# Kernel tuning notes

Hardware: AMD Instinct MI355X
Metric: run time of the kernel (lower is better)

Reference implementation:

```python
import jax, jax.numpy as jnp
import numpy as np

N_NODES = 100000
N_EDGES = 1600000
IN_CH, HID_CH, OUT_CH = 128, 128, 64


def glorot(key, fan_in, fan_out):
    lim = np.sqrt(6.0 / (fan_in + fan_out)).astype(np.float32)
    return jax.random.uniform(key, (fan_in, fan_out), jnp.float32, -lim, lim)


def gcn_conv(x, src, dst, W, b):
    """PyG GCNConv: add self-loops, symmetric deg^-1/2 normalization,
    linear transform, scatter-add aggregation at targets, plus bias."""
    n = x.shape[0]
    xw = x @ W  # [N, F_out]
    loop = jnp.arange(n)
    s = jnp.concatenate([src, loop])  # sources (message origin)
    d = jnp.concatenate([dst, loop])  # targets (aggregation site)
    deg = jax.ops.segment_sum(jnp.ones_like(d, dtype=xw.dtype), d, num_segments=n)
    dinv = jnp.where(deg > 0, jax.lax.rsqrt(deg), 0.0)
    norm = dinv[s] * dinv[d]  # [E+N]
    out = jax.ops.segment_sum(norm[:, None] * xw[s], d, num_segments=n)
    return out + b


def setup_inputs() -> dict:
    key = jax.random.key(0)
    ks = jax.random.split(key, 8)
    x = jax.random.normal(ks[0], (N_NODES, IN_CH), jnp.float32)
    edge_index = jax.random.randint(ks[1], (2, N_EDGES), 0, N_NODES, jnp.int64)
    return {
        "x": x,
        "edge_index": edge_index,
        "W1": glorot(ks[2], IN_CH, HID_CH),
        "b1": jnp.zeros((HID_CH,), jnp.float32),
        "W2": glorot(ks[3], HID_CH, HID_CH),
        "b2": jnp.zeros((HID_CH,), jnp.float32),
        "W3": glorot(ks[4], HID_CH, OUT_CH),
        "b3": jnp.zeros((OUT_CH,), jnp.float32),
    }


def reference(x, edge_index, W1, b1, W2, b2, W3, b3):
    src, dst = edge_index[0], edge_index[1]
    # eval mode: dropout is identity
    h = jax.nn.relu(gcn_conv(x, src, dst, W1, b1))
    h = jax.nn.relu(gcn_conv(h, src, dst, W2, b2))
    h = gcn_conv(h, src, dst, W3, b3)
    return jax.nn.log_softmax(h, axis=1)
```

## Files before the change

kernel.cpp:

```cpp
#include <hip/hip_runtime.h>
#include <math.h>


#define NN 100000
#define NE 1600000
#define NBUK 391
#define BCAP 4608

typedef float floatx4 __attribute__((ext_vector_type(4)));
typedef short short8 __attribute__((ext_vector_type(8)));

__device__ __forceinline__ unsigned short f2bf(float f) {
    unsigned u = __float_as_uint(f);
    unsigned r = (u + 0x7fffu + ((u >> 16) & 1u)) >> 16;
    return (unsigned short)r;
}
__device__ __forceinline__ float bflo(unsigned u) { return __uint_as_float(u << 16); }
__device__ __forceinline__ float bfhi(unsigned u) { return __uint_as_float(u & 0xffff0000u); }

__global__ __launch_bounds__(256) void k_wprep_all(const float* __restrict__ W1, const float* __restrict__ W2,
                                                   const float* __restrict__ W3,
                                                   unsigned short* __restrict__ wt1, unsigned short* __restrict__ wt2,
                                                   unsigned short* __restrict__ wt3) {
    int idx = blockIdx.x * 256 + threadIdx.x;
    if (idx < 16384) {
        int n = idx >> 7, k = idx & 127;
        wt1[idx] = f2bf(W1[k * 128 + n]);
    } else if (idx < 32768) {
        int i = idx - 16384;
        int n = i >> 7, k = i & 127;
        wt2[i] = f2bf(W2[k * 128 + n]);
    } else if (idx < 40960) {
        int i = idx - 32768;
        int n = i >> 7, k = i & 127;
        wt3[i] = f2bf(W3[k * 64 + n]);
    }
}

__global__ __launch_bounds__(256) void k_bucket(const int4* __restrict__ src4, const int4* __restrict__ dst4,
                                                int* __restrict__ bcur, int* __restrict__ bbuf, int E) {
    __shared__ int hist[NBUK];
    __shared__ int base[NBUK];
    int t = threadIdx.x;
    for (int b = t; b < NBUK; b += 256) hist[b] = 0;
    __syncthreads();
    int E4 = E >> 2;
    int q0 = blockIdx.x * 1024;
    int4 sv[4], dv[4];
    bool valid[4];
    #pragma unroll
    for (int j = 0; j < 4; j++) {
        int q = q0 + j * 256 + t;
        valid[j] = (q < E4);
        if (valid[j]) {
            sv[j] = src4[q];
            dv[j] = dst4[q];
            atomicAdd(&hist[dv[j].x >> 8], 1);
            atomicAdd(&hist[dv[j].y >> 8], 1);
            atomicAdd(&hist[dv[j].z >> 8], 1);
            atomicAdd(&hist[dv[j].w >> 8], 1);
        }
    }
    __syncthreads();
    for (int b = t; b < NBUK; b += 256) {
        int c = hist[b];
        base[b] = c ? atomicAdd(&bcur[b], c) : 0;
        hist[b] = 0;
    }
    __syncthreads();
    #pragma unroll
    for (int j = 0; j < 4; j++) {
        if (valid[j]) {
            int ss[4] = {sv[j].x, sv[j].y, sv[j].z, sv[j].w};
            int dd[4] = {dv[j].x, dv[j].y, dv[j].z, dv[j].w};
            #pragma unroll
            for (int u = 0; u < 4; u++) {
                int b = dd[u] >> 8;
                int r = atomicAdd(&hist[b], 1);
                int pos = base[b] + r;
                if (pos < BCAP) bbuf[b * BCAP + pos] = (ss[u] << 8) | (dd[u] & 255);
            }
        }
    }
}

__global__ void k_scanbuckets(const int* __restrict__ bcur, int* __restrict__ bbase, int nb,
                              int* __restrict__ row_ptr, int n, int E) {
    int lane = threadIdx.x;
    int carry = 0;
    for (int base = 0; base < nb; base += 64) {
        int idx = base + lane;
        int v = (idx < nb) ? min(bcur[idx], BCAP) : 0;
        int orig = v;
        #pragma unroll
        for (int o = 1; o < 64; o <<= 1) {
            int u = __shfl_up(v, o);
            if (lane >= o) v += u;
        }
        if (idx < nb) bbase[idx] = carry + v - orig;
        carry += __shfl(v, 63);
    }
    if (lane == 0) row_ptr[n] = E;
}

__global__ __launch_bounds__(256) void k_build(const int* __restrict__ bcur, const int* __restrict__ bbase,
                                               const int* __restrict__ bbuf,
                                               int* __restrict__ row_ptr, int* __restrict__ csr,
                                               float* __restrict__ dinv, int N) {
    __shared__ int sh[256];
    __shared__ int cur[256];
    __shared__ int loc[BCAP];
    int b = blockIdx.x, t = threadIdx.x;
    int cnt = min(bcur[b], BCAP);
    int gbase = bbase[b];
    const int* bp = bbuf + b * BCAP;
    sh[t] = 0;
    __syncthreads();
    for (int i = t; i < cnt; i += 256) atomicAdd(&sh[bp[i] & 255], 1);
    __syncthreads();
    int v = sh[t];
    for (int o = 1; o < 256; o <<= 1) {
        int u = (t >= o) ? sh[t - o] : 0;
        __syncthreads();
        sh[t] += u;
        __syncthreads();
    }
    int excl = sh[t] - v;
    int node = b * 256 + t;
    if (node < N) {
        row_ptr[node] = gbase + excl;
        dinv[node] = rsqrtf((float)v + 1.0f);
    }
    cur[t] = excl;
    __syncthreads();
    for (int i = t; i < cnt; i += 256) {
        int p = bp[i];
        int r = atomicAdd(&cur[p & 255], 1);
        loc[r] = p >> 8;
    }
    __syncthreads();
    for (int i = t; i < cnt; i += 256) csr[gbase + i] = loc[i];
}


template <int NC, bool CVT>
__global__ __launch_bounds__(256) void k_mfma(const void* __restrict__ Av, const unsigned short* __restrict__ Wtg,
                                              const float* __restrict__ dinv, unsigned short* __restrict__ Y, int M) {
    constexpr int K = 128;
    constexpr int NT = NC / 16;
    constexpr int NU = NC / 32;
    __shared__ unsigned short Wt[NC][136];
    __shared__ unsigned short Ost[4][16][NC + 8];
    int t = threadIdx.x;
    for (int idx = t; idx < NC * 16; idx += 256) {
        int nrow = idx >> 4, chunk = idx & 15;
        *(uint4*)&Wt[nrow][chunk * 8] = *(const uint4*)(Wtg + nrow * K + chunk * 8);
    }
    __syncthreads();
    int lane = t & 63, wid = t >> 6;
    int col = lane & 15, quad = lane >> 4;
    int nstrips = M / 16;
    int stride = gridDim.x * 4;
    int s = blockIdx.x * 4 + wid;
    if (s >= nstrips) return;

    auto loadA = [&](int strip, short8 af[4]) {
        int row0 = strip * 16;
        if (CVT) {
            const float* Af = (const float*)Av + (size_t)(row0 + col) * K + quad * 8;
            #pragma unroll
            for (int ks = 0; ks < 4; ks++) {
                float4 f0 = *(const float4*)(Af + ks * 32);
                float4 f1 = *(const float4*)(Af + ks * 32 + 4);
                short8 v;
                v[0] = (short)f2bf(f0.x); v[1] = (short)f2bf(f0.y); v[2] = (short)f2bf(f0.z); v[3] = (short)f2bf(f0.w);
                v[4] = (short)f2bf(f1.x); v[5] = (short)f2bf(f1.y); v[6] = (short)f2bf(f1.z); v[7] = (short)f2bf(f1.w);
                af[ks] = v;
            }
        } else {
            const unsigned short* Ab = (const unsigned short*)Av + (size_t)(row0 + col) * K + quad * 8;
            #pragma unroll
            for (int ks = 0; ks < 4; ks++) af[ks] = *(const short8*)(Ab + ks * 32);
        }
    };

    short8 cur[4];
    loadA(s, cur);
    while (true) {
        int snext = s + stride;
        bool has = (snext < nstrips);
        short8 nxt[4];
        if (has) loadA(snext, nxt);

        floatx4 acc[NT];
        #pragma unroll
        for (int i = 0; i < NT; i++) acc[i] = (floatx4){0.f, 0.f, 0.f, 0.f};
        #pragma unroll
        for (int ks = 0; ks < 4; ks++) {
            #pragma unroll
            for (int nt = 0; nt < NT; nt++) {
                short8 bfrag = *(const short8*)&Wt[nt * 16 + col][ks * 32 + quad * 8];
                acc[nt] = __builtin_amdgcn_mfma_f32_16x16x32_bf16(cur[ks], bfrag, acc[nt], 0, 0, 0);
            }
        }
        int row0 = s * 16;
        #pragma unroll
        for (int r = 0; r < 4; r++) {
            float dv = dinv[row0 + quad * 4 + r];
            #pragma unroll
            for (int nt = 0; nt < NT; nt++)
                Ost[wid][quad * 4 + r][nt * 16 + col] = f2bf(acc[nt][r] * dv);
        }
        #pragma unroll
        for (int i = 0; i < NU; i++) {
            int idx = i * 64 + lane;
            int rr = (NC == 128) ? (idx >> 4) : (idx >> 3);
            int cc = (NC == 128) ? (idx & 15) : (idx & 7);
            ((uint4*)&Y[(size_t)(row0 + rr) * NC])[cc] = *(uint4*)&Ost[wid][rr][cc * 8];
        }
        if (!has) break;
        s = snext;
        #pragma unroll
        for (int ks = 0; ks < 4; ks++) cur[ks] = nxt[ks];
    }
}


__device__ __forceinline__ void acc8(float* a, uint4 v) {
    a[0] += bflo(v.x); a[1] += bfhi(v.x);
    a[2] += bflo(v.y); a[3] += bfhi(v.y);
    a[4] += bflo(v.z); a[5] += bfhi(v.z);
    a[6] += bflo(v.w); a[7] += bfhi(v.w);
}

__global__ __launch_bounds__(256) void k_gather_relu_bf(const uint4* __restrict__ y, const int* __restrict__ csr,
                                                        const int* __restrict__ row_ptr, const float* __restrict__ dinv,
                                                        const float* __restrict__ bias, uint4* __restrict__ h, int n) {
    int half = blockIdx.x & 1;
    int node = (blockIdx.x >> 1) * 32 + (threadIdx.x >> 3);
    int c = (threadIdx.x & 7) + half * 8;
    if (node >= n) return;
    int s0 = row_ptr[node], s1 = row_ptr[node + 1];
    float a[8] = {};
    acc8(a, y[(size_t)node * 16 + c]);
    int p = s0;
    for (; p + 4 <= s1; p += 4) {
        int i0 = csr[p], i1 = csr[p + 1], i2 = csr[p + 2], i3 = csr[p + 3];
        uint4 v0 = y[(size_t)i0 * 16 + c];
        uint4 v1 = y[(size_t)i1 * 16 + c];
        uint4 v2 = y[(size_t)i2 * 16 + c];
        uint4 v3 = y[(size_t)i3 * 16 + c];
        acc8(a, v0); acc8(a, v1); acc8(a, v2); acc8(a, v3);
    }
    for (; p < s1; p++) acc8(a, y[(size_t)csr[p] * 16 + c]);
    float s = dinv[node];
    float4 b0 = ((const float4*)bias)[c * 2];
    float4 b1 = ((const float4*)bias)[c * 2 + 1];
    float r0 = fmaxf(s * a[0] + b0.x, 0.f), r1 = fmaxf(s * a[1] + b0.y, 0.f);
    float r2 = fmaxf(s * a[2] + b0.z, 0.f), r3 = fmaxf(s * a[3] + b0.w, 0.f);
    float r4 = fmaxf(s * a[4] + b1.x, 0.f), r5 = fmaxf(s * a[5] + b1.y, 0.f);
    float r6 = fmaxf(s * a[6] + b1.z, 0.f), r7 = fmaxf(s * a[7] + b1.w, 0.f);
    uint4 o;
    o.x = ((unsigned)f2bf(r1) << 16) | f2bf(r0);
    o.y = ((unsigned)f2bf(r3) << 16) | f2bf(r2);
    o.z = ((unsigned)f2bf(r5) << 16) | f2bf(r4);
    o.w = ((unsigned)f2bf(r7) << 16) | f2bf(r6);
    h[(size_t)node * 16 + c] = o;
}

__global__ __launch_bounds__(256) void k_gather_lsm_bf(const uint4* __restrict__ y, const int* __restrict__ csr,
                                                       const int* __restrict__ row_ptr, const float* __restrict__ dinv,
                                                       const float* __restrict__ bias, float4* __restrict__ out4, int n) {
    int node = blockIdx.x * 32 + (threadIdx.x >> 3);
    int c = threadIdx.x & 7;
    if (node >= n) return;
    int s0 = row_ptr[node], s1 = row_ptr[node + 1];
    float a[8] = {};
    acc8(a, y[(size_t)node * 8 + c]);
    int p = s0;
    for (; p + 4 <= s1; p += 4) {
        int i0 = csr[p], i1 = csr[p + 1], i2 = csr[p + 2], i3 = csr[p + 3];
        uint4 v0 = y[(size_t)i0 * 8 + c];
        uint4 v1 = y[(size_t)i1 * 8 + c];
        uint4 v2 = y[(size_t)i2 * 8 + c];
        uint4 v3 = y[(size_t)i3 * 8 + c];
        acc8(a, v0); acc8(a, v1); acc8(a, v2); acc8(a, v3);
    }
    for (; p < s1; p++) acc8(a, y[(size_t)csr[p] * 8 + c]);
    float s = dinv[node];
    float4 b0 = ((const float4*)bias)[c * 2];
    float4 b1 = ((const float4*)bias)[c * 2 + 1];
    float v[8];
    v[0] = s * a[0] + b0.x; v[1] = s * a[1] + b0.y; v[2] = s * a[2] + b0.z; v[3] = s * a[3] + b0.w;
    v[4] = s * a[4] + b1.x; v[5] = s * a[5] + b1.y; v[6] = s * a[6] + b1.z; v[7] = s * a[7] + b1.w;
    float m = v[0];
    #pragma unroll
    for (int i = 1; i < 8; i++) m = fmaxf(m, v[i]);
    #pragma unroll
    for (int o = 4; o > 0; o >>= 1) m = fmaxf(m, __shfl_xor(m, o));
    float sum = 0.f;
    #pragma unroll
    for (int i = 0; i < 8; i++) sum += expf(v[i] - m);
    #pragma unroll
    for (int o = 4; o > 0; o >>= 1) sum += __shfl_xor(sum, o);
    float lse = m + logf(sum);
    out4[(size_t)node * 16 + c * 2]     = make_float4(v[0] - lse, v[1] - lse, v[2] - lse, v[3] - lse);
    out4[(size_t)node * 16 + c * 2 + 1] = make_float4(v[4] - lse, v[5] - lse, v[6] - lse, v[7] - lse);
}


extern "C" void kernel_launch(void* const* d_in, const int* in_sizes, int n_in,
                              void* d_out, int out_size, void* d_ws, size_t ws_size,
                              hipStream_t stream) {
    const float* x  = (const float*)d_in[0];
    const int*   ei = (const int*)d_in[1];
    const float* W1 = (const float*)d_in[2];
    const float* b1 = (const float*)d_in[3];
    const float* W2 = (const float*)d_in[4];
    const float* b2 = (const float*)d_in[5];
    const float* W3 = (const float*)d_in[6];
    const float* b3 = (const float*)d_in[7];
    float* out = (float*)d_out;

    const int N = NN, E = NE;

    char* ws = (char*)d_ws;
    size_t off = 0;
    auto alloc = [&](size_t bytes) -> void* {
        void* p = ws + off;
        off += bytes;
        off = (off + 255) & ~(size_t)255;
        return p;
    };
    int*            row_ptr = (int*)alloc((size_t)(N + 1) * 4);
    float*          dinvv   = (float*)alloc((size_t)N * 4);
    int*            bcur    = (int*)alloc(512 * 4);
    int*            bbase   = (int*)alloc(512 * 4);
    int*            bbuf    = (int*)alloc((size_t)NBUK * BCAP * 4);
    int*            csr     = (int*)alloc((size_t)E * 4);
    unsigned short* wt1     = (unsigned short*)alloc(128 * 128 * 2);
    unsigned short* wt2     = (unsigned short*)alloc(128 * 128 * 2);
    unsigned short* wt3     = (unsigned short*)alloc(64 * 128 * 2);
    unsigned short* yb      = (unsigned short*)alloc((size_t)N * 128 * 2);
    unsigned short* hb      = (unsigned short*)alloc((size_t)N * 128 * 2);
    (void)ws_size; (void)in_sizes; (void)n_in; (void)out_size;

    const int* srcp = ei;
    const int* dstp = ei + E;

    hipMemsetAsync(bcur, 0, 512 * 4, stream);
    k_wprep_all<<<160, 256, 0, stream>>>(W1, W2, W3, wt1, wt2, wt3);
    k_bucket<<<(E + 4095) / 4096, 256, 0, stream>>>((const int4*)srcp, (const int4*)dstp, bcur, bbuf, E);
    k_scanbuckets<<<1, 64, 0, stream>>>(bcur, bbase, NBUK, row_ptr, N, E);
    k_build<<<NBUK, 256, 0, stream>>>(bcur, bbase, bbuf, row_ptr, csr, dinvv, N);

    k_mfma<128, true><<<768, 256, 0, stream>>>(x, wt1, dinvv, yb, N);
    k_gather_relu_bf<<<(N / 32) * 2, 256, 0, stream>>>((const uint4*)yb, csr, row_ptr, dinvv, b1, (uint4*)hb, N);
    k_mfma<128, false><<<768, 256, 0, stream>>>(hb, wt2, dinvv, yb, N);
    k_gather_relu_bf<<<(N / 32) * 2, 256, 0, stream>>>((const uint4*)yb, csr, row_ptr, dinvv, b2, (uint4*)hb, N);
    k_mfma<64, false><<<768, 256, 0, stream>>>(hb, wt3, dinvv, yb, N);
    k_gather_lsm_bf<<<N / 32, 256, 0, stream>>>((const uint4*)yb, csr, row_ptr, dinvv, b3, (float4*)out, N);
}
```

Baseline: 326.6 us.

## Sort nodes by in-degree and order CSR neighbors by source range

Replaces the bucket scan and CSR build with a degree histogram, a counting sort of nodes by in-degree into a permutation, and a CSR build whose row pointers follow the permuted slot order. Inside each row, neighbors are grouped by the high bits of the source index. The gather kernels now iterate over slots and map each one back to its node through perm. The aim is to give wavefronts uniform trip counts and to make neighbor reads more cache-local. In exchange it adds several small preprocessing kernels and global atomics, output writes become scattered, and degrees above 255 would overflow the histogram.

```diff
diff --git a/kernel.cpp b/kernel.cpp
--- a/kernel.cpp
+++ b/kernel.cpp
@@ -84,62 +84,107 @@
     }
 }
 
-__global__ void k_scanbuckets(const int* __restrict__ bcur, int* __restrict__ bbase, int nb,
-                              int* __restrict__ row_ptr, int n, int E) {
-    int lane = threadIdx.x;
-    int carry = 0;
-    for (int base = 0; base < nb; base += 64) {
-        int idx = base + lane;
-        int v = (idx < nb) ? min(bcur[idx], BCAP) : 0;
-        int orig = v;
-        #pragma unroll
-        for (int o = 1; o < 64; o <<= 1) {
-            int u = __shfl_up(v, o);
-            if (lane >= o) v += u;
-        }
-        if (idx < nb) bbase[idx] = carry + v - orig;
-        carry += __shfl(v, 63);
-    }
-    if (lane == 0) row_ptr[n] = E;
-}
-
-__global__ __launch_bounds__(256) void k_build(const int* __restrict__ bcur, const int* __restrict__ bbase,
-                                               const int* __restrict__ bbuf,
-                                               int* __restrict__ row_ptr, int* __restrict__ csr,
-                                               float* __restrict__ dinv, int N) {
+__global__ __launch_bounds__(256) void k_hist(const int* __restrict__ bcur, const int* __restrict__ bbuf,
+                                              int* __restrict__ deg, float* __restrict__ dinv,
+                                              int* __restrict__ dhist, int N) {
     __shared__ int sh[256];
-    __shared__ int cur[256];
-    __shared__ int loc[BCAP];
+    __shared__ int lh[256];
     int b = blockIdx.x, t = threadIdx.x;
     int cnt = min(bcur[b], BCAP);
-    int gbase = bbase[b];
     const int* bp = bbuf + b * BCAP;
-    sh[t] = 0;
+    sh[t] = 0; lh[t] = 0;
     __syncthreads();
     for (int i = t; i < cnt; i += 256) atomicAdd(&sh[bp[i] & 255], 1);
     __syncthreads();
-    int v = sh[t];
-    for (int o = 1; o < 256; o <<= 1) {
-        int u = (t >= o) ? sh[t - o] : 0;
-        __syncthreads();
-        sh[t] += u;
-        __syncthreads();
-    }
-    int excl = sh[t] - v;
     int node = b * 256 + t;
+    int d = sh[t];
     if (node < N) {
-        row_ptr[node] = gbase + excl;
-        dinv[node] = rsqrtf((float)v + 1.0f);
-    }
-    cur[t] = excl;
+        deg[node] = d;
+        dinv[node] = rsqrtf((float)d + 1.0f);
+        atomicAdd(&lh[min(d, 255)], 1);
+    }
+    __syncthreads();
+    if (lh[t]) atomicAdd(&dhist[t], lh[t]);
+}
+
+__global__ void k_permhist(const int* __restrict__ dhist, int* __restrict__ dbase, int* __restrict__ wsum,
+                           int* __restrict__ dcur, int* __restrict__ row_ptr, int N, int E) {
+    if (threadIdx.x == 0) {
+        int run = 0, wrun = 0;
+        for (int d = 0; d < 256; d++) {
+            dbase[d] = run; dcur[d] = run; wsum[d] = wrun;
+            int h = dhist[d];
+            run += h; wrun += d * h;
+        }
+        row_ptr[N] = E;
+    }
+}
+
+__global__ __launch_bounds__(256) void k_permscatter(const int* __restrict__ deg, int* __restrict__ dcur,
+                                                     const int* __restrict__ dbase, const int* __restrict__ wsum,
+                                                     int* __restrict__ perm, int* __restrict__ islot,
+                                                     int* __restrict__ row_ptr, int N) {
+    __shared__ int lh[256], lbase[256], lcur[256];
+    int t = threadIdx.x;
+    int node = blockIdx.x * 256 + t;
+    lh[t] = 0; lcur[t] = 0;
+    __syncthreads();
+    int d = -1;
+    if (node < N) { d = deg[node]; atomicAdd(&lh[d], 1); }
+    __syncthreads();
+    if (lh[t]) lbase[t] = atomicAdd(&dcur[t], lh[t]);
+    __syncthreads();
+    if (node < N) {
+        int r = atomicAdd(&lcur[d], 1);
+        int slot = lbase[d] + r;
+        perm[slot] = node;
+        islot[node] = slot;
+        row_ptr[slot] = wsum[d] + (slot - dbase[d]) * d;
+    }
+}
+
+__global__ __launch_bounds__(256) void k_csr(const int* __restrict__ bcur, const int* __restrict__ bbuf,
+                                             const int* __restrict__ row_ptr, const int* __restrict__ islot,
+                                             int* __restrict__ csr, int N) {
+    __shared__ int sh[4096];
+    __shared__ int cur[4096];
+    __shared__ int tot[256];
+    __shared__ int rp[256];
+    int b = blockIdx.x, t = threadIdx.x;
+    int cnt = min(bcur[b], BCAP);
+    const int* bp = bbuf + b * BCAP;
+    for (int k = t; k < 4096; k += 256) sh[k] = 0;
     __syncthreads();
     for (int i = t; i < cnt; i += 256) {
         int p = bp[i];
-        int r = atomicAdd(&cur[p & 255], 1);
-        loc[r] = p >> 8;
-    }
-    __syncthreads();
-    for (int i = t; i < cnt; i += 256) csr[gbase + i] = loc[i];
+        int key = ((p & 255) << 4) | (int)((unsigned)(p >> 8) >> 13);
+        atomicAdd(&sh[key], 1);
+    }
+    __syncthreads();
+    int run = 0;
+    #pragma unroll
+    for (int j = 0; j < 16; j++) run += sh[t * 16 + j];
+    tot[t] = run;
+    __syncthreads();
+    for (int o = 1; o < 256; o <<= 1) {
+        int u = (t >= o) ? tot[t - o] : 0;
+        __syncthreads();
+        tot[t] += u;
+        __syncthreads();
+    }
+    int excl = tot[t] - run;
+    int base = excl;
+    #pragma unroll
+    for (int j = 0; j < 16; j++) { cur[t * 16 + j] = base; base += sh[t * 16 + j]; }
+    int node = b * 256 + t;
+    if (node < N) rp[t] = row_ptr[islot[node]] - excl;
+    __syncthreads();
+    for (int i = t; i < cnt; i += 256) {
+        int p = bp[i];
+        int key = ((p & 255) << 4) | (int)((unsigned)(p >> 8) >> 13);
+        int r = atomicAdd(&cur[key], 1);
+        csr[rp[p & 255] + r] = p >> 8;
+    }
 }
 
 
@@ -234,13 +279,15 @@
 }
 
 __global__ __launch_bounds__(256) void k_gather_relu_bf(const uint4* __restrict__ y, const int* __restrict__ csr,
-                                                        const int* __restrict__ row_ptr, const float* __restrict__ dinv,
+                                                        const int* __restrict__ row_ptr, const int* __restrict__ perm,
+                                                        const float* __restrict__ dinv,
                                                         const float* __restrict__ bias, uint4* __restrict__ h, int n) {
     int half = blockIdx.x & 1;
-    int node = (blockIdx.x >> 1) * 32 + (threadIdx.x >> 3);
+    int slot = (blockIdx.x >> 1) * 32 + (threadIdx.x >> 3);
     int c = (threadIdx.x & 7) + half * 8;
-    if (node >= n) return;
-    int s0 = row_ptr[node], s1 = row_ptr[node + 1];
+    if (slot >= n) return;
+    int node = perm[slot];
+    int s0 = row_ptr[slot], s1 = row_ptr[slot + 1];
     float a[8] = {};
     acc8(a, y[(size_t)node * 16 + c]);
     int p = s0;
@@ -269,12 +316,14 @@
 }
 
 __global__ __launch_bounds__(256) void k_gather_lsm_bf(const uint4* __restrict__ y, const int* __restrict__ csr,
-                                                       const int* __restrict__ row_ptr, const float* __restrict__ dinv,
+                                                       const int* __restrict__ row_ptr, const int* __restrict__ perm,
+                                                       const float* __restrict__ dinv,
                                                        const float* __restrict__ bias, float4* __restrict__ out4, int n) {
-    int node = blockIdx.x * 32 + (threadIdx.x >> 3);
+    int slot = blockIdx.x * 32 + (threadIdx.x >> 3);
     int c = threadIdx.x & 7;
-    if (node >= n) return;
-    int s0 = row_ptr[node], s1 = row_ptr[node + 1];
+    if (slot >= n) return;
+    int node = perm[slot];
+    int s0 = row_ptr[slot], s1 = row_ptr[slot + 1];
     float a[8] = {};
     acc8(a, y[(size_t)node * 8 + c]);
     int p = s0;
@@ -335,9 +384,15 @@
     int*            row_ptr = (int*)alloc((size_t)(N + 1) * 4);
     float*          dinvv   = (float*)alloc((size_t)N * 4);
     int*            bcur    = (int*)alloc(512 * 4);
-    int*            bbase   = (int*)alloc(512 * 4);
+    int*            dhist   = (int*)alloc(256 * 4);
+    int*            dbase   = (int*)alloc(256 * 4);
+    int*            wsum    = (int*)alloc(256 * 4);
+    int*            dcur    = (int*)alloc(256 * 4);
     int*            bbuf    = (int*)alloc((size_t)NBUK * BCAP * 4);
     int*            csr     = (int*)alloc((size_t)E * 4);
+    int*            deg     = (int*)alloc((size_t)N * 4);
+    int*            perm    = (int*)alloc((size_t)N * 4);
+    int*            islot   = (int*)alloc((size_t)N * 4);
     unsigned short* wt1     = (unsigned short*)alloc(128 * 128 * 2);
     unsigned short* wt2     = (unsigned short*)alloc(128 * 128 * 2);
     unsigned short* wt3     = (unsigned short*)alloc(64 * 128 * 2);
@@ -348,16 +403,18 @@
     const int* srcp = ei;
     const int* dstp = ei + E;
 
-    hipMemsetAsync(bcur, 0, 512 * 4, stream);
+    hipMemsetAsync(bcur, 0, (512 + 256) * 4, stream);
     k_wprep_all<<<160, 256, 0, stream>>>(W1, W2, W3, wt1, wt2, wt3);
     k_bucket<<<(E + 4095) / 4096, 256, 0, stream>>>((const int4*)srcp, (const int4*)dstp, bcur, bbuf, E);
-    k_scanbuckets<<<1, 64, 0, stream>>>(bcur, bbase, NBUK, row_ptr, N, E);
-    k_build<<<NBUK, 256, 0, stream>>>(bcur, bbase, bbuf, row_ptr, csr, dinvv, N);
+    k_hist<<<NBUK, 256, 0, stream>>>(bcur, bbuf, deg, dinvv, dhist, N);
+    k_permhist<<<1, 64, 0, stream>>>(dhist, dbase, wsum, dcur, row_ptr, N, E);
+    k_permscatter<<<(N + 255) / 256, 256, 0, stream>>>(deg, dcur, dbase, wsum, perm, islot, row_ptr, N);
+    k_csr<<<NBUK, 256, 0, stream>>>(bcur, bbuf, row_ptr, islot, csr, N);
 
     k_mfma<128, true><<<768, 256, 0, stream>>>(x, wt1, dinvv, yb, N);
-    k_gather_relu_bf<<<(N / 32) * 2, 256, 0, stream>>>((const uint4*)yb, csr, row_ptr, dinvv, b1, (uint4*)hb, N);
+    k_gather_relu_bf<<<(N / 32) * 2, 256, 0, stream>>>((const uint4*)yb, csr, row_ptr, perm, dinvv, b1, (uint4*)hb, N);
     k_mfma<128, false><<<768, 256, 0, stream>>>(hb, wt2, dinvv, yb, N);
-    k_gather_relu_bf<<<(N / 32) * 2, 256, 0, stream>>>((const uint4*)yb, csr, row_ptr, dinvv, b2, (uint4*)hb, N);
+    k_gather_relu_bf<<<(N / 32) * 2, 256, 0, stream>>>((const uint4*)yb, csr, row_ptr, perm, dinvv, b2, (uint4*)hb, N);
     k_mfma<64, false><<<768, 256, 0, stream>>>(hb, wt3, dinvv, yb, N);
-    k_gather_lsm_bf<<<N / 32, 256, 0, stream>>>((const uint4*)yb, csr, row_ptr, dinvv, b3, (float4*)out, N);
-}
+    k_gather_lsm_bf<<<N / 32, 256, 0, stream>>>((const uint4*)yb, csr, row_ptr, perm, dinvv, b3, (float4*)out, N);
+}
```

Result: slower. 344.5 us (+5.5%).

## Partition CSR neighbor lists by source chunk and gather chunk-by-chunk for L2 locality

Applied to the files above, without the earlier changes.

The CSR build now sorts each node's neighbors by source-index chunk (src>>14, 7 chunks) and stores 8 per-node chunk offsets instead of a single row pointer. The gather kernels hold several nodes per thread (4 for the ReLU layers, 2 for log-softmax) with a reduced grid, and walk all their nodes through chunk 0, then chunk 1, and so on. The intent is to keep the randomly accessed feature rows inside a smaller source window at any moment, so more of the gather reads hit L2. The costs are an 8x larger row-pointer array, extra shared-memory histogram work in the build, loss of the 4-way unrolled neighbor loop, and no global synchronization to keep blocks aligned on the same chunk.

```diff
diff --git a/kernel.cpp b/kernel.cpp
--- a/kernel.cpp
+++ b/kernel.cpp
@@ -6,6 +6,7 @@
 #define NE 1600000
 #define NBUK 391
 #define BCAP 4608
+#define NCH 7
 
 typedef float floatx4 __attribute__((ext_vector_type(4)));
 typedef short short8 __attribute__((ext_vector_type(8)));
@@ -84,8 +85,7 @@
     }
 }
 
-__global__ void k_scanbuckets(const int* __restrict__ bcur, int* __restrict__ bbase, int nb,
-                              int* __restrict__ row_ptr, int n, int E) {
+__global__ void k_scanbuckets(const int* __restrict__ bcur, int* __restrict__ bbase, int nb) {
     int lane = threadIdx.x;
     int carry = 0;
     for (int base = 0; base < nb; base += 64) {
@@ -100,42 +100,54 @@
         if (idx < nb) bbase[idx] = carry + v - orig;
         carry += __shfl(v, 63);
     }
-    if (lane == 0) row_ptr[n] = E;
 }
 
 __global__ __launch_bounds__(256) void k_build(const int* __restrict__ bcur, const int* __restrict__ bbase,
                                                const int* __restrict__ bbuf,
-                                               int* __restrict__ row_ptr, int* __restrict__ csr,
+                                               int* __restrict__ rpc, int* __restrict__ csr,
                                                float* __restrict__ dinv, int N) {
-    __shared__ int sh[256];
-    __shared__ int cur[256];
+    __shared__ int sh[2048];
+    __shared__ int cur[2048];
+    __shared__ int tot[256];
     __shared__ int loc[BCAP];
     int b = blockIdx.x, t = threadIdx.x;
     int cnt = min(bcur[b], BCAP);
     int gbase = bbase[b];
     const int* bp = bbuf + b * BCAP;
-    sh[t] = 0;
-    __syncthreads();
-    for (int i = t; i < cnt; i += 256) atomicAdd(&sh[bp[i] & 255], 1);
-    __syncthreads();
-    int v = sh[t];
-    for (int o = 1; o < 256; o <<= 1) {
-        int u = (t >= o) ? sh[t - o] : 0;
-        __syncthreads();
-        sh[t] += u;
-        __syncthreads();
-    }
-    int excl = sh[t] - v;
-    int node = b * 256 + t;
-    if (node < N) {
-        row_ptr[node] = gbase + excl;
-        dinv[node] = rsqrtf((float)v + 1.0f);
-    }
-    cur[t] = excl;
+    for (int k = t; k < 2048; k += 256) sh[k] = 0;
     __syncthreads();
     for (int i = t; i < cnt; i += 256) {
         int p = bp[i];
-        int r = atomicAdd(&cur[p & 255], 1);
+        int key = ((p & 255) << 3) | (int)((unsigned)p >> 22);
+        atomicAdd(&sh[key], 1);
+    }
+    __syncthreads();
+    int run = 0;
+    #pragma unroll
+    for (int j = 0; j < 8; j++) run += sh[t * 8 + j];
+    tot[t] = run;
+    __syncthreads();
+    for (int o = 1; o < 256; o <<= 1) {
+        int u = (t >= o) ? tot[t - o] : 0;
+        __syncthreads();
+        tot[t] += u;
+        __syncthreads();
+    }
+    int excl = tot[t] - run;
+    int node = b * 256 + t;
+    int base = excl;
+    #pragma unroll
+    for (int j = 0; j < 8; j++) {
+        if (node < N) rpc[node * 8 + j] = gbase + base;
+        cur[t * 8 + j] = base;
+        base += sh[t * 8 + j];
+    }
+    if (node < N) dinv[node] = rsqrtf((float)run + 1.0f);
+    __syncthreads();
+    for (int i = t; i < cnt; i += 256) {
+        int p = bp[i];
+        int key = ((p & 255) << 3) | (int)((unsigned)p >> 22);
+        int r = atomicAdd(&cur[key], 1);
         loc[r] = p >> 8;
     }
     __syncthreads();
@@ -233,79 +245,106 @@
     a[6] += bflo(v.w); a[7] += bfhi(v.w);
 }
 
-__global__ __launch_bounds__(256) void k_gather_relu_bf(const uint4* __restrict__ y, const int* __restrict__ csr,
-                                                        const int* __restrict__ row_ptr, const float* __restrict__ dinv,
-                                                        const float* __restrict__ bias, uint4* __restrict__ h, int n) {
+#define GRELU_GRID 1564
+__global__ __launch_bounds__(256, 7) void k_gather_relu_bf(const uint4* __restrict__ y, const int* __restrict__ csr,
+                                                           const int* __restrict__ rpc,
+                                                           const float* __restrict__ dinv,
+                                                           const float* __restrict__ bias, uint4* __restrict__ h, int n) {
     int half = blockIdx.x & 1;
-    int node = (blockIdx.x >> 1) * 32 + (threadIdx.x >> 3);
-    int c = (threadIdx.x & 7) + half * 8;
-    if (node >= n) return;
-    int s0 = row_ptr[node], s1 = row_ptr[node + 1];
-    float a[8] = {};
-    acc8(a, y[(size_t)node * 16 + c]);
-    int p = s0;
-    for (; p + 4 <= s1; p += 4) {
-        int i0 = csr[p], i1 = csr[p + 1], i2 = csr[p + 2], i3 = csr[p + 3];
-        uint4 v0 = y[(size_t)i0 * 16 + c];
-        uint4 v1 = y[(size_t)i1 * 16 + c];
-        uint4 v2 = y[(size_t)i2 * 16 + c];
-        uint4 v3 = y[(size_t)i3 * 16 + c];
-        acc8(a, v0); acc8(a, v1); acc8(a, v2); acc8(a, v3);
-    }
-    for (; p < s1; p++) acc8(a, y[(size_t)csr[p] * 16 + c]);
-    float s = dinv[node];
-    float4 b0 = ((const float4*)bias)[c * 2];
-    float4 b1 = ((const float4*)bias)[c * 2 + 1];
-    float r0 = fmaxf(s * a[0] + b0.x, 0.f), r1 = fmaxf(s * a[1] + b0.y, 0.f);
-    float r2 = fmaxf(s * a[2] + b0.z, 0.f), r3 = fmaxf(s * a[3] + b0.w, 0.f);
-    float r4 = fmaxf(s * a[4] + b1.x, 0.f), r5 = fmaxf(s * a[5] + b1.y, 0.f);
-    float r6 = fmaxf(s * a[6] + b1.z, 0.f), r7 = fmaxf(s * a[7] + b1.w, 0.f);
-    uint4 o;
-    o.x = ((unsigned)f2bf(r1) << 16) | f2bf(r0);
-    o.y = ((unsigned)f2bf(r3) << 16) | f2bf(r2);
-    o.z = ((unsigned)f2bf(r5) << 16) | f2bf(r4);
-    o.w = ((unsigned)f2bf(r7) << 16) | f2bf(r6);
-    h[(size_t)node * 16 + c] = o;
-}
-
-__global__ __launch_bounds__(256) void k_gather_lsm_bf(const uint4* __restrict__ y, const int* __restrict__ csr,
-                                                       const int* __restrict__ row_ptr, const float* __restrict__ dinv,
-                                                       const float* __restrict__ bias, float4* __restrict__ out4, int n) {
-    int node = blockIdx.x * 32 + (threadIdx.x >> 3);
+    int gh = blockIdx.x >> 1;
+    int it = threadIdx.x >> 3;
+    int cidx = (threadIdx.x & 7) + half * 8;
+    int nodes[4];
+    int s0g[4];
+    float a[4][8] = {};
+    #pragma unroll
+    for (int j = 0; j < 4; j++) {
+        int node = (gh + j * 782) * 32 + it;
+        nodes[j] = (node < n) ? node : -1;
+        s0g[j] = (node < n) ? rpc[node * 8] : 0;
+    }
+    for (int c = 0; c < NCH; c++) {
+        #pragma unroll
+        for (int j = 0; j < 4; j++) {
+            int node = nodes[j];
+            if (node < 0) continue;
+            int s1 = rpc[node * 8 + c + 1];
+            if (c == (node >> 14)) acc8(a[j], y[(size_t)node * 16 + cidx]);
+            for (int p = s0g[j]; p < s1; p++) acc8(a[j], y[(size_t)csr[p] * 16 + cidx]);
+            s0g[j] = s1;
+        }
+    }
+    #pragma unroll
+    for (int j = 0; j < 4; j++) {
+        int node = nodes[j];
+        if (node < 0) continue;
+        float s = dinv[node];
+        float4 b0 = ((const float4*)bias)[cidx * 2];
+        float4 b1 = ((const float4*)bias)[cidx * 2 + 1];
+        float r0 = fmaxf(s * a[j][0] + b0.x, 0.f), r1 = fmaxf(s * a[j][1] + b0.y, 0.f);
+        float r2 = fmaxf(s * a[j][2] + b0.z, 0.f), r3 = fmaxf(s * a[j][3] + b0.w, 0.f);
+        float r4 = fmaxf(s * a[j][4] + b1.x, 0.f), r5 = fmaxf(s * a[j][5] + b1.y, 0.f);
+        float r6 = fmaxf(s * a[j][6] + b1.z, 0.f), r7 = fmaxf(s * a[j][7] + b1.w, 0.f);
+        uint4 o;
+        o.x = ((unsigned)f2bf(r1) << 16) | f2bf(r0);
+        o.y = ((unsigned)f2bf(r3) << 16) | f2bf(r2);
+        o.z = ((unsigned)f2bf(r5) << 16) | f2bf(r4);
+        o.w = ((unsigned)f2bf(r7) << 16) | f2bf(r6);
+        h[(size_t)node * 16 + cidx] = o;
+    }
+}
+
+#define GLSM_GRID 1564
+__global__ __launch_bounds__(256, 7) void k_gather_lsm_bf(const uint4* __restrict__ y, const int* __restrict__ csr,
+                                                          const int* __restrict__ rpc,
+                                                          const float* __restrict__ dinv,
+                                                          const float* __restrict__ bias, float4* __restrict__ out4, int n) {
+    int it = threadIdx.x >> 3;
     int c = threadIdx.x & 7;
-    if (node >= n) return;
-    int s0 = row_ptr[node], s1 = row_ptr[node + 1];
-    float a[8] = {};
-    acc8(a, y[(size_t)node * 8 + c]);
-    int p = s0;
-    for (; p + 4 <= s1; p += 4) {
-        int i0 = csr[p], i1 = csr[p + 1], i2 = csr[p + 2], i3 = csr[p + 3];
-        uint4 v0 = y[(size_t)i0 * 8 + c];
-        uint4 v1 = y[(size_t)i1 * 8 + c];
-        uint4 v2 = y[(size_t)i2 * 8 + c];
-        uint4 v3 = y[(size_t)i3 * 8 + c];
-        acc8(a, v0); acc8(a, v1); acc8(a, v2); acc8(a, v3);
-    }
-    for (; p < s1; p++) acc8(a, y[(size_t)csr[p] * 8 + c]);
-    float s = dinv[node];
-    float4 b0 = ((const float4*)bias)[c * 2];
-    float4 b1 = ((const float4*)bias)[c * 2 + 1];
-    float v[8];
-    v[0] = s * a[0] + b0.x; v[1] = s * a[1] + b0.y; v[2] = s * a[2] + b0.z; v[3] = s * a[3] + b0.w;
-    v[4] = s * a[4] + b1.x; v[5] = s * a[5] + b1.y; v[6] = s * a[6] + b1.z; v[7] = s * a[7] + b1.w;
-    float m = v[0];
-    #pragma unroll
-    for (int i = 1; i < 8; i++) m = fmaxf(m, v[i]);
-    #pragma unroll
-    for (int o = 4; o > 0; o >>= 1) m = fmaxf(m, __shfl_xor(m, o));
-    float sum = 0.f;
-    #pragma unroll
-    for (int i = 0; i < 8; i++) sum += expf(v[i] - m);
-    #pragma unroll
-    for (int o = 4; o > 0; o >>= 1) sum += __shfl_xor(sum, o);
-    float lse = m + logf(sum);
-    out4[(size_t)node * 16 + c * 2]     = make_float4(v[0] - lse, v[1] - lse, v[2] - lse, v[3] - lse);
-    out4[(size_t)node * 16 + c * 2 + 1] = make_float4(v[4] - lse, v[5] - lse, v[6] - lse, v[7] - lse);
+    int nodes[2];
+    int s0g[2];
+    float a[2][8] = {};
+    #pragma unroll
+    for (int j = 0; j < 2; j++) {
+        int node = (blockIdx.x + j * GLSM_GRID) * 32 + it;
+        nodes[j] = (node < n) ? node : -1;
+        s0g[j] = (node < n) ? rpc[node * 8] : 0;
+    }
+    for (int ch = 0; ch < NCH; ch++) {
+        #pragma unroll
+        for (int j = 0; j < 2; j++) {
+            int node = nodes[j];
+            if (node < 0) continue;
+            int s1 = rpc[node * 8 + ch + 1];
+            if (ch == (node >> 14)) acc8(a[j], y[(size_t)node * 8 + c]);
+            for (int p = s0g[j]; p < s1; p++) acc8(a[j], y[(size_t)csr[p] * 8 + c]);
+            s0g[j] = s1;
+        }
+    }
+    #pragma unroll
+    for (int j = 0; j < 2; j++) {
+        int node = nodes[j];
+        if (node < 0) continue;
+        float s = dinv[node];
+        float4 b0 = ((const float4*)bias)[c * 2];
+        float4 b1 = ((const float4*)bias)[c * 2 + 1];
+        float v[8];
+        v[0] = s * a[j][0] + b0.x; v[1] = s * a[j][1] + b0.y; v[2] = s * a[j][2] + b0.z; v[3] = s * a[j][3] + b0.w;
+        v[4] = s * a[j][4] + b1.x; v[5] = s * a[j][5] + b1.y; v[6] = s * a[j][6] + b1.z; v[7] = s * a[j][7] + b1.w;
+        float m = v[0];
+        #pragma unroll
+        for (int i = 1; i < 8; i++) m = fmaxf(m, v[i]);
+        #pragma unroll
+        for (int o = 4; o > 0; o >>= 1) m = fmaxf(m, __shfl_xor(m, o));
+        float sum = 0.f;
+        #pragma unroll
+        for (int i = 0; i < 8; i++) sum += expf(v[i] - m);
+        #pragma unroll
+        for (int o = 4; o > 0; o >>= 1) sum += __shfl_xor(sum, o);
+        float lse = m + logf(sum);
+        out4[(size_t)node * 16 + c * 2]     = make_float4(v[0] - lse, v[1] - lse, v[2] - lse, v[3] - lse);
+        out4[(size_t)node * 16 + c * 2 + 1] = make_float4(v[4] - lse, v[5] - lse, v[6] - lse, v[7] - lse);
+    }
 }
 
 
@@ -332,7 +371,7 @@
         off = (off + 255) & ~(size_t)255;
         return p;
     };
-    int*            row_ptr = (int*)alloc((size_t)(N + 1) * 4);
+    int*            rpc     = (int*)alloc((size_t)(N * 8 + 8) * 4);
     float*          dinvv   = (float*)alloc((size_t)N * 4);
     int*            bcur    = (int*)alloc(512 * 4);
     int*            bbase   = (int*)alloc(512 * 4);
@@ -351,13 +390,13 @@
     hipMemsetAsync(bcur, 0, 512 * 4, stream);
     k_wprep_all<<<160, 256, 0, stream>>>(W1, W2, W3, wt1, wt2, wt3);
     k_bucket<<<(E + 4095) / 4096, 256, 0, stream>>>((const int4*)srcp, (const int4*)dstp, bcur, bbuf, E);
-    k_scanbuckets<<<1, 64, 0, stream>>>(bcur, bbase, NBUK, row_ptr, N, E);
-    k_build<<<NBUK, 256, 0, stream>>>(bcur, bbase, bbuf, row_ptr, csr, dinvv, N);
+    k_scanbuckets<<<1, 64, 0, stream>>>(bcur, bbase, NBUK);
+    k_build<<<NBUK, 256, 0, stream>>>(bcur, bbase, bbuf, rpc, csr, dinvv, N);
 
     k_mfma<128, true><<<768, 256, 0, stream>>>(x, wt1, dinvv, yb, N);
-    k_gather_relu_bf<<<(N / 32) * 2, 256, 0, stream>>>((const uint4*)yb, csr, row_ptr, dinvv, b1, (uint4*)hb, N);
+    k_gather_relu_bf<<<GRELU_GRID, 256, 0, stream>>>((const uint4*)yb, csr, rpc, dinvv, b1, (uint4*)hb, N);
     k_mfma<128, false><<<768, 256, 0, stream>>>(hb, wt2, dinvv, yb, N);
-    k_gather_relu_bf<<<(N / 32) * 2, 256, 0, stream>>>((const uint4*)yb, csr, row_ptr, dinvv, b2, (uint4*)hb, N);
+    k_gather_relu_bf<<<GRELU_GRID, 256, 0, stream>>>((const uint4*)yb, csr, rpc, dinvv, b2, (uint4*)hb, N);
     k_mfma<64, false><<<768, 256, 0, stream>>>(hb, wt3, dinvv, yb, N);
-    k_gather_lsm_bf<<<N / 32, 256, 0, stream>>>((const uint4*)yb, csr, row_ptr, dinvv, b3, (float4*)out, N);
-}
+    k_gather_lsm_bf<<<GLSM_GRID, 256, 0, stream>>>((const uint4*)yb, csr, rpc, dinvv, b3, (float4*)out, N);
+}
```

Result: slower. 455.7 us (+39.5%).
